# Kernel optimization log

Measured on AMD Instinct MI355X. Metric: run time of the kernel, lower is better.

Reference implementation:

```python
import jax, jax.numpy as jnp
import numpy as np

N_NODES = 50000
IN_DIM = 128
HIDDEN = 64
OUT_DIM = 3
HEADS1 = 4
NEG_SLOPE = 0.2
EPS = 1e-16


def _glorot(key, shape):
    fan_in, fan_out = shape[0], shape[-1]
    lim = (6.0 / (fan_in + fan_out)) ** 0.5
    return jax.random.uniform(key, shape, jnp.float32, -lim, lim)


def setup_inputs() -> dict:
    key = jax.random.key(0)
    ks = jax.random.split(key, 12)
    x = jax.random.normal(ks[0], (N_NODES, IN_DIM), jnp.float32)
    edge_index = jax.random.randint(ks[1], (2, 400000), 0, N_NODES, jnp.int64)
    # layer 1: GATConv(in=128, out=64, heads=4)
    W1 = _glorot(ks[2], (IN_DIM, HEADS1 * HIDDEN))
    att_src1 = _glorot(ks[3], (HEADS1, HIDDEN))
    att_dst1 = _glorot(ks[4], (HEADS1, HIDDEN))
    b1 = jnp.zeros((HEADS1 * HIDDEN,), jnp.float32)
    # layer 2: GATConv(in=256, out=64, heads=1)
    W2 = _glorot(ks[5], (HEADS1 * HIDDEN, HIDDEN))
    att_src2 = _glorot(ks[6], (1, HIDDEN))
    att_dst2 = _glorot(ks[7], (1, HIDDEN))
    b2 = jnp.zeros((HIDDEN,), jnp.float32)
    # output linear
    Wout = _glorot(ks[8], (HIDDEN, OUT_DIM))
    bout = jnp.zeros((OUT_DIM,), jnp.float32)
    return {"x": x, "edge_index": edge_index, "W1": W1, "att_src1": att_src1,
            "att_dst1": att_dst1, "b1": b1, "W2": W2, "att_src2": att_src2,
            "att_dst2": att_dst2, "b2": b2, "Wout": Wout, "bout": bout}


def gat_conv(x, src, dst, W, a_src, a_dst, b, n_nodes):
    H, C = a_src.shape
    h = (x @ W).reshape(n_nodes, H, C)            # [N,H,C]
    a_s = jnp.sum(h * a_src[None], axis=-1)        # [N,H]
    a_d = jnp.sum(h * a_dst[None], axis=-1)        # [N,H]
    e = jax.nn.leaky_relu(a_s[src] + a_d[dst], NEG_SLOPE)  # [E,H]
    # segment softmax over incoming edges of each dst node
    m = jax.ops.segment_max(e, dst, num_segments=n_nodes)
    ex = jnp.exp(e - m[dst])
    denom = jax.ops.segment_sum(ex, dst, num_segments=n_nodes)
    alpha = ex / (denom[dst] + EPS)                # [E,H]
    msg = h[src] * alpha[..., None]                # [E,H,C]
    out = jax.ops.segment_sum(msg, dst, num_segments=n_nodes)
    return out.reshape(n_nodes, H * C) + b


def reference(x, edge_index, W1, att_src1, att_dst1, b1, W2, att_src2, att_dst2, b2, Wout, bout):
    n = x.shape[0]
    loop = jnp.arange(n, dtype=edge_index.dtype)
    src = jnp.concatenate([edge_index[0], loop])   # add self loops (PyG default)
    dst = jnp.concatenate([edge_index[1], loop])
    h = gat_conv(x, src, dst, W1, att_src1, att_dst1, b1, n)
    h = jax.nn.elu(h)
    h = gat_conv(h, src, dst, W2, att_src2, att_dst2, b2, n)
    h = jax.nn.elu(h)
    return h @ Wout + bout
```

## Files before the change

kernel.cpp:

```cpp
#include <hip/hip_runtime.h>
#include <hip/hip_bf16.h>
#include <math.h>

#define N_NODES  50000
#define IN_DIM   128
#define HIDDEN   64
#define OUT_DIM  3
#define HEADS1   4
#define E_RAW    400000
#define E_TOT    450000
#define NEG_SLOPE 0.2f
#define WPREP_BLOCKS 128
#define EB_SC ((E_TOT + 255) / 256)
#define MB_GE (N_NODES / 16)

typedef __attribute__((ext_vector_type(8))) short bf16x8;
typedef __attribute__((ext_vector_type(4))) float f32x4;

static __device__ __forceinline__ float bfu(unsigned short u) {
    return __uint_as_float(((unsigned)u) << 16);
}
static __device__ __forceinline__ unsigned short f2b_bits(float v) {
    __hip_bfloat16 b = __float2bfloat16(v);
    return *reinterpret_cast<unsigned short*>(&b);
}

static __device__ __forceinline__ void get_edge(const int* __restrict__ ei, int is64,
                                                int e, int& s, int& d) {
    if (e >= E_RAW) { s = d = e - E_RAW; return; }
    if (is64) { s = ei[2 * e]; d = ei[2 * E_RAW + 2 * e]; }
    else      { s = ei[e];     d = ei[E_RAW + e]; }
    s = min(max(s, 0), N_NODES - 1);
    d = min(max(d, 0), N_NODES - 1);
}

static __device__ __forceinline__ int block_is64(const int* __restrict__ ei,
                                                 int e, bool valid, int* nzbuf) {
    bool real = valid && (e < E_RAW);
    int hv = real ? ei[2 * e + 1] : 0;
    if (threadIdx.x == 0) *nzbuf = 0;
    __syncthreads();
    if (__any(hv != 0) && (threadIdx.x & 63) == 0) *nzbuf = 1;
    __syncthreads();
    return (*nzbuf == 0);
}

__global__ void wprep_count_kernel(const float* __restrict__ W1, __hip_bfloat16* __restrict__ W1T,
                                   const float* __restrict__ W2, __hip_bfloat16* __restrict__ W2T,
                                   const int* __restrict__ ei, int* __restrict__ deg) {
    __shared__ int nz;
    int bid = blockIdx.x;
    if (bid < WPREP_BLOCKS) {
        int i = bid * 256 + threadIdx.x;
        if (i < 256 * 128) {
            int n = i >> 7, k = i & 127;
            *((unsigned short*)W1T + i) = f2b_bits(W1[k * 256 + n]);
        }
        if (i < 64 * 256) {
            int n = i >> 8, k = i & 255;
            *((unsigned short*)W2T + i) = f2b_bits(W2[k * 64 + n]);
        }
        return;
    }
    int e = (bid - WPREP_BLOCKS) * 256 + threadIdx.x;
    bool valid = e < E_TOT;
    int is64 = block_is64(ei, e, valid, &nz);
    if (!valid) return;
    int s, d;
    get_edge(ei, is64, e, s, d);
    atomicAdd(&deg[d], 1);
}

__global__ void scan_all_kernel(const int* __restrict__ deg, int* __restrict__ row_ptr,
                                int* __restrict__ cursor) {
    __shared__ int wsum[4];
    const int t = threadIdx.x, wv = t >> 6, ln = t & 63;
    int carry = 0;
    if (t == 0) row_ptr[0] = 0;
    for (int chunk = 0; chunk < 49; ++chunk) {
        int g = chunk * 256 + t;
        int4 d = (g < 12500) ? ((const int4*)deg)[g] : make_int4(0, 0, 0, 0);
        int p0 = d.x, p1 = p0 + d.y, p2 = p1 + d.z, p3 = p2 + d.w;
        int s = p3;
        #pragma unroll
        for (int off = 1; off < 64; off <<= 1) {
            int u = __shfl_up(s, off, 64);
            if (ln >= off) s += u;
        }
        if (ln == 63) wsum[wv] = s;
        __syncthreads();
        int wbase = carry;
        #pragma unroll
        for (int w = 0; w < 4; w++) wbase += (w < wv) ? wsum[w] : 0;
        int ex = wbase + s - p3;
        if (g < 12500) {
            int i = g * 4;
            row_ptr[i + 1] = ex + p0; row_ptr[i + 2] = ex + p1;
            row_ptr[i + 3] = ex + p2; row_ptr[i + 4] = ex + p3;
            cursor[i]     = ex;       cursor[i + 1]  = ex + p0;
            cursor[i + 2] = ex + p1;  cursor[i + 3]  = ex + p2;
        }
        carry += wsum[0] + wsum[1] + wsum[2] + wsum[3];
        __syncthreads();
    }
}

__global__ void __launch_bounds__(256) scatter_gemm_l1_kernel(
        const int* __restrict__ ei,
        int* __restrict__ cursor, int* __restrict__ csr_src,
        const float* __restrict__ x, const __hip_bfloat16* __restrict__ W1T,
        const float* __restrict__ att_s, const float* __restrict__ att_d,
        __hip_bfloat16* __restrict__ h1,
        float* __restrict__ asb4, float* __restrict__ adb4) {
    __shared__ unsigned short As[16][136];
    __shared__ int nz;
    if (blockIdx.x < EB_SC) {
        int e = blockIdx.x * 256 + threadIdx.x;
        bool valid = e < E_TOT;
        int is64 = block_is64(ei, e, valid, &nz);
        if (!valid) return;
        int s, d;
        get_edge(ei, is64, e, s, d);
        int pos = atomicAdd(&cursor[d], 1);
        csr_src[pos] = s;
        return;
    }
    const int tid = threadIdx.x;
    const int wave = tid >> 6, lane = tid & 63;
    const int quad = lane >> 4, m = lane & 15;
    const int row0 = (blockIdx.x - EB_SC) * 16;
    {
        int r = tid >> 4, seg = tid & 15;
        const float* xa = x + (size_t)(row0 + r) * IN_DIM + seg * 8;
        float4 u = *(const float4*)xa;
        float4 v = *(const float4*)(xa + 4);
        ushort4 p0, p1;
        p0.x = f2b_bits(u.x); p0.y = f2b_bits(u.y); p0.z = f2b_bits(u.z); p0.w = f2b_bits(u.w);
        p1.x = f2b_bits(v.x); p1.y = f2b_bits(v.y); p1.z = f2b_bits(v.z); p1.w = f2b_bits(v.w);
        *(ushort4*)&As[r][seg * 8]     = p0;
        *(ushort4*)&As[r][seg * 8 + 4] = p1;
    }
    __syncthreads();
    const int n0w = wave * 64;
    f32x4 acc0 = {0.f, 0.f, 0.f, 0.f}, acc1 = acc0, acc2 = acc0, acc3 = acc0;
    #pragma unroll
    for (int k0 = 0; k0 < IN_DIM; k0 += 32) {
        int kk = k0 + quad * 8;
        bf16x8 a = *(const bf16x8*)&As[m][kk];
        bf16x8 b0 = *(const bf16x8*)(W1T + (size_t)(n0w +  0 + m) * IN_DIM + kk);
        bf16x8 b1 = *(const bf16x8*)(W1T + (size_t)(n0w + 16 + m) * IN_DIM + kk);
        bf16x8 b2 = *(const bf16x8*)(W1T + (size_t)(n0w + 32 + m) * IN_DIM + kk);
        bf16x8 b3 = *(const bf16x8*)(W1T + (size_t)(n0w + 48 + m) * IN_DIM + kk);
        acc0 = __builtin_amdgcn_mfma_f32_16x16x32_bf16(a, b0, acc0, 0, 0, 0);
        acc1 = __builtin_amdgcn_mfma_f32_16x16x32_bf16(a, b1, acc1, 0, 0, 0);
        acc2 = __builtin_amdgcn_mfma_f32_16x16x32_bf16(a, b2, acc2, 0, 0, 0);
        acc3 = __builtin_amdgcn_mfma_f32_16x16x32_bf16(a, b3, acc3, 0, 0, 0);
    }
    float ats0 = att_s[n0w +  0 + m], atd0 = att_d[n0w +  0 + m];
    float ats1 = att_s[n0w + 16 + m], atd1 = att_d[n0w + 16 + m];
    float ats2 = att_s[n0w + 32 + m], atd2 = att_d[n0w + 32 + m];
    float ats3 = att_s[n0w + 48 + m], atd3 = att_d[n0w + 48 + m];
    unsigned short* out = (unsigned short*)h1;
    #pragma unroll
    for (int i = 0; i < 4; i++) {
        int grow = row0 + quad * 4 + i;
        size_t base = (size_t)grow * 256;
        out[base + n0w +  0 + m] = f2b_bits(acc0[i]);
        out[base + n0w + 16 + m] = f2b_bits(acc1[i]);
        out[base + n0w + 32 + m] = f2b_bits(acc2[i]);
        out[base + n0w + 48 + m] = f2b_bits(acc3[i]);
        float ps = acc0[i] * ats0 + acc1[i] * ats1 + acc2[i] * ats2 + acc3[i] * ats3;
        float pd = acc0[i] * atd0 + acc1[i] * atd1 + acc2[i] * atd2 + acc3[i] * atd3;
        #pragma unroll
        for (int off = 1; off < 16; off <<= 1) {
            ps += __shfl_xor(ps, off, 16);
            pd += __shfl_xor(pd, off, 16);
        }
        if (m == 0) {
            asb4[grow * 4 + wave] = ps;
            adb4[grow * 4 + wave] = pd;
        }
    }
}

__global__ void __launch_bounds__(256) gat_gather4_kernel(
        const int* __restrict__ row_ptr, const int* __restrict__ csr_src,
        const float* __restrict__ asb4, const float* __restrict__ adb4,
        const __hip_bfloat16* __restrict__ h1, const float* __restrict__ bias,
        __hip_bfloat16* __restrict__ eluagg) {
    int wave = threadIdx.x >> 6;
    int lane = threadIdx.x & 63;
    int n = blockIdx.x * 4 + wave;
    if (n >= N_NODES) return;
    int b = row_ptr[n], e = row_ptr[n + 1];
    const int c    = lane & 31;
    const int slot = lane >> 5;
    const int head = c >> 3;
    const int ei   = lane >> 2;
    const int hh   = lane & 3;
    float adnh = adb4[n * 4 + hh];
    float acc[8];
    #pragma unroll
    for (int i = 0; i < 8; i++) acc[i] = 0.f;
    float l = 0.f;
    for (int c0 = b; c0 < e; c0 += 16) {
        int cnt = min(16, e - c0);
        int s_all = (lane < cnt) ? csr_src[c0 + lane] : 0;
        int sE = __shfl(s_all, ei, 64);
        float w_all = 0.f;
        if (ei < cnt) {
            float v = asb4[sE * 4 + hh] + adnh;
            v = (v > 0.f) ? v : NEG_SLOPE * v;
            w_all = __expf(v);
        }
        #pragma unroll 2
        for (int k = 0; k < cnt; k += 2) {
            int eidx = k + slot;
            int s = __shfl(s_all, eidx, 64);
            float w = __shfl(w_all, eidx * 4 + head, 64);
            bf16x8 f = *(const bf16x8*)(h1 + (size_t)s * 256 + c * 8);
            l += w;
            #pragma unroll
            for (int i = 0; i < 8; i++)
                acc[i] += w * bfu((unsigned short)f[i]);
        }
    }
    #pragma unroll
    for (int i = 0; i < 8; i++) acc[i] += __shfl_xor(acc[i], 32, 64);
    l += __shfl_xor(l, 32, 64);
    if (lane < 32) {
        float il = 1.f / (l + 1e-16f);
        float4 b0 = *(const float4*)(bias + c * 8);
        float4 b1 = *(const float4*)(bias + c * 8 + 4);
        float r[8];
        r[0] = acc[0] * il + b0.x; r[1] = acc[1] * il + b0.y;
        r[2] = acc[2] * il + b0.z; r[3] = acc[3] * il + b0.w;
        r[4] = acc[4] * il + b1.x; r[5] = acc[5] * il + b1.y;
        r[6] = acc[6] * il + b1.z; r[7] = acc[7] * il + b1.w;
        bf16x8 st;
        #pragma unroll
        for (int i = 0; i < 8; i++) {
            float v = (r[i] > 0.f) ? r[i] : expm1f(r[i]);
            st[i] = (short)f2b_bits(v);
        }
        *(bf16x8*)(eluagg + (size_t)n * 256 + c * 8) = st;
    }
}

__global__ void __launch_bounds__(256) gemm_l2_mfma_kernel(
        const __hip_bfloat16* __restrict__ eluagg, const __hip_bfloat16* __restrict__ W2T,
        const float* __restrict__ att_s, const float* __restrict__ att_d,
        __hip_bfloat16* __restrict__ h2,
        float* __restrict__ asb, float* __restrict__ adb) {
    __shared__ float sPS[4][16];
    __shared__ float sPD[4][16];
    const int tid = threadIdx.x;
    const int wave = tid >> 6, lane = tid & 63;
    const int quad = lane >> 4, m = lane & 15;
    const int row0 = blockIdx.x * 16;
    const int n0 = wave * 16;
    f32x4 acc = {0.f, 0.f, 0.f, 0.f};
    #pragma unroll
    for (int k0 = 0; k0 < 256; k0 += 32) {
        int kk = k0 + quad * 8;
        bf16x8 a = *(const bf16x8*)(eluagg + (size_t)(row0 + m) * 256 + kk);
        bf16x8 b = *(const bf16x8*)(W2T + (size_t)(n0 + m) * 256 + kk);
        acc = __builtin_amdgcn_mfma_f32_16x16x32_bf16(a, b, acc, 0, 0, 0);
    }
    float ats = att_s[n0 + m], atd = att_d[n0 + m];
    unsigned short* out = (unsigned short*)h2;
    #pragma unroll
    for (int i = 0; i < 4; i++) {
        int grow = row0 + quad * 4 + i;
        out[(size_t)grow * 64 + n0 + m] = f2b_bits(acc[i]);
        float ps = acc[i] * ats;
        float pd = acc[i] * atd;
        #pragma unroll
        for (int off = 1; off < 16; off <<= 1) {
            ps += __shfl_xor(ps, off, 16);
            pd += __shfl_xor(pd, off, 16);
        }
        if (m == 0) {
            sPS[wave][quad * 4 + i] = ps;
            sPD[wave][quad * 4 + i] = pd;
        }
    }
    __syncthreads();
    if (tid < 16) {
        float ps = sPS[0][tid] + sPS[1][tid] + sPS[2][tid] + sPS[3][tid];
        float pd = sPD[0][tid] + sPD[1][tid] + sPD[2][tid] + sPD[3][tid];
        asb[row0 + tid] = ps;
        adb[row0 + tid] = pd;
    }
}

__global__ void __launch_bounds__(256) gat_gather1_out_kernel(
        const int* __restrict__ row_ptr, const int* __restrict__ csr_src,
        const float* __restrict__ asb, const float* __restrict__ adb,
        const __hip_bfloat16* __restrict__ h2, const float* __restrict__ bias,
        const float* __restrict__ Wout, const float* __restrict__ bout,
        float* __restrict__ out) {
    int wave = threadIdx.x >> 6;
    int lane = threadIdx.x & 63;
    int n = blockIdx.x * 4 + wave;
    if (n >= N_NODES) return;
    int b = row_ptr[n], e = row_ptr[n + 1];
    const int c    = lane & 7;
    const int slot = lane >> 3;
    float adn = adb[n];
    float acc[8];
    #pragma unroll
    for (int i = 0; i < 8; i++) acc[i] = 0.f;
    float l = 0.f;
    for (int c0 = b; c0 < e; c0 += 64) {
        int cnt = min(64, e - c0);
        int s_all = (lane < cnt) ? csr_src[c0 + lane] : 0;
        float w_all = 0.f;
        if (lane < cnt) {
            float v = asb[s_all] + adn;
            v = (v > 0.f) ? v : NEG_SLOPE * v;
            w_all = __expf(v);
        }
        #pragma unroll 2
        for (int k = 0; k < cnt; k += 8) {
            int eidx = k + slot;
            int s = __shfl(s_all, eidx, 64);
            float w = __shfl(w_all, eidx, 64);
            bf16x8 f = *(const bf16x8*)(h2 + (size_t)s * 64 + c * 8);
            l += w;
            #pragma unroll
            for (int i = 0; i < 8; i++)
                acc[i] += w * bfu((unsigned short)f[i]);
        }
    }
    #pragma unroll
    for (int off = 8; off < 64; off <<= 1) {
        #pragma unroll
        for (int i = 0; i < 8; i++) acc[i] += __shfl_xor(acc[i], off, 64);
        l += __shfl_xor(l, off, 64);
    }
    float il = 1.f / (l + 1e-16f);
    float4 b0 = *(const float4*)(bias + c * 8);
    float4 b1 = *(const float4*)(bias + c * 8 + 4);
    float v[8];
    v[0] = acc[0] * il + b0.x; v[1] = acc[1] * il + b0.y;
    v[2] = acc[2] * il + b0.z; v[3] = acc[3] * il + b0.w;
    v[4] = acc[4] * il + b1.x; v[5] = acc[5] * il + b1.y;
    v[6] = acc[6] * il + b1.z; v[7] = acc[7] * il + b1.w;
    #pragma unroll
    for (int i = 0; i < 8; i++) v[i] = (v[i] > 0.f) ? v[i] : expm1f(v[i]);
    const float* wp = Wout + c * 24;
    float o0 = 0.f, o1 = 0.f, o2 = 0.f;
    #pragma unroll
    for (int i = 0; i < 8; i++) {
        o0 += v[i] * wp[i * 3 + 0];
        o1 += v[i] * wp[i * 3 + 1];
        o2 += v[i] * wp[i * 3 + 2];
    }
    #pragma unroll
    for (int off = 1; off < 8; off <<= 1) {
        o0 += __shfl_xor(o0, off, 64);
        o1 += __shfl_xor(o1, off, 64);
        o2 += __shfl_xor(o2, off, 64);
    }
    if (lane == 0) {
        out[n * OUT_DIM + 0] = o0 + bout[0];
        out[n * OUT_DIM + 1] = o1 + bout[1];
        out[n * OUT_DIM + 2] = o2 + bout[2];
    }
}

extern "C" void kernel_launch(void* const* d_in, const int* in_sizes, int n_in,
                              void* d_out, int out_size, void* d_ws, size_t ws_size,
                              hipStream_t stream) {
    const float* x    = (const float*)d_in[0];
    const int*   ei   = (const int*)d_in[1];
    const float* W1   = (const float*)d_in[2];
    const float* as1  = (const float*)d_in[3];
    const float* ad1  = (const float*)d_in[4];
    const float* b1   = (const float*)d_in[5];
    const float* W2   = (const float*)d_in[6];
    const float* as2  = (const float*)d_in[7];
    const float* ad2  = (const float*)d_in[8];
    const float* b2v  = (const float*)d_in[9];
    const float* Wout = (const float*)d_in[10];
    const float* bout = (const float*)d_in[11];
    float* out = (float*)d_out;

    float* ws    = (float*)d_ws;
    float* asb4  = ws + 16;
    float* adb4  = asb4 + (size_t)N_NODES * 4;
    float* asb1  = adb4 + (size_t)N_NODES * 4;
    float* adb1  = asb1 + N_NODES;
    __hip_bfloat16* h1     = (__hip_bfloat16*)(adb1 + N_NODES);
    __hip_bfloat16* eluagg = (__hip_bfloat16*)(h1 + (size_t)N_NODES * 256);
    __hip_bfloat16* h2     = (__hip_bfloat16*)(eluagg + (size_t)N_NODES * 256);
    __hip_bfloat16* W1T    = (__hip_bfloat16*)(h2 + (size_t)N_NODES * 64);
    __hip_bfloat16* W2T    = W1T + 256 * 128;
    int* deg     = (int*)(W2T + 64 * 256);
    int* row_ptr = deg + N_NODES;
    int* cursor  = row_ptr + N_NODES + 16;
    int* csr_src = cursor + N_NODES;

    const int EB = EB_SC;
    const int AB = (N_NODES + 3) / 4;

    hipMemsetAsync(deg, 0, (size_t)N_NODES * sizeof(int), stream);
    wprep_count_kernel<<<WPREP_BLOCKS + EB, 256, 0, stream>>>(W1, W1T, W2, W2T, ei, deg);
    scan_all_kernel<<<1, 256, 0, stream>>>(deg, row_ptr, cursor);

    scatter_gemm_l1_kernel<<<EB + MB_GE, 256, 0, stream>>>(ei, cursor, csr_src,
                                                           x, W1T, as1, ad1, h1, asb4, adb4);

    gat_gather4_kernel<<<AB, 256, 0, stream>>>(row_ptr, csr_src, asb4, adb4, h1, b1, eluagg);

    gemm_l2_mfma_kernel<<<MB_GE, 256, 0, stream>>>(eluagg, W2T, as2, ad2, h2, asb1, adb1);

    gat_gather1_out_kernel<<<AB, 256, 0, stream>>>(row_ptr, csr_src, asb1, adb1, h2,
                                                   b2v, Wout, bout, out);
}
```

Baseline: 297.3 us.

## Fuse layer-1 gather with layer-2 GEMM, parallelize scan, stage GEMM stores in LDS

Layer-1 attention aggregation and the layer-2 MFMA GEMM now run in one 1024-thread kernel: 16 waves each aggregate one node into LDS, then four waves run the GEMM from LDS. This removes the round trip of the 50000x256 bf16 eluagg buffer through global memory. The single-block prefix scan becomes a 49-block scan where each block re-sums the earlier degree chunks, and both GEMM epilogues stage results in LDS so they can be written with coalesced 16-byte stores. The cost is larger blocks, a barrier per block and idle waves during the GEMM phase.

```diff
diff --git a/kernel.cpp b/kernel.cpp
--- a/kernel.cpp
+++ b/kernel.cpp
@@ -10,6 +10,7 @@
 #define E_RAW    400000
 #define E_TOT    450000
 #define NEG_SLOPE 0.2f
+#define N_CHUNKS 49
 #define WPREP_BLOCKS 128
 #define EB_SC ((E_TOT + 255) / 256)
 #define MB_GE (N_NODES / 16)
@@ -71,38 +72,47 @@
     atomicAdd(&deg[d], 1);
 }
 
-__global__ void scan_all_kernel(const int* __restrict__ deg, int* __restrict__ row_ptr,
-                                int* __restrict__ cursor) {
+__global__ void scan_fused_kernel(const int* __restrict__ deg, int* __restrict__ row_ptr,
+                                  int* __restrict__ cursor) {
     __shared__ int wsum[4];
-    const int t = threadIdx.x, wv = t >> 6, ln = t & 63;
-    int carry = 0;
-    if (t == 0) row_ptr[0] = 0;
-    for (int chunk = 0; chunk < 49; ++chunk) {
-        int g = chunk * 256 + t;
-        int4 d = (g < 12500) ? ((const int4*)deg)[g] : make_int4(0, 0, 0, 0);
-        int p0 = d.x, p1 = p0 + d.y, p2 = p1 + d.z, p3 = p2 + d.w;
-        int s = p3;
-        #pragma unroll
-        for (int off = 1; off < 64; off <<= 1) {
-            int u = __shfl_up(s, off, 64);
-            if (ln >= off) s += u;
-        }
-        if (ln == 63) wsum[wv] = s;
-        __syncthreads();
-        int wbase = carry;
-        #pragma unroll
-        for (int w = 0; w < 4; w++) wbase += (w < wv) ? wsum[w] : 0;
-        int ex = wbase + s - p3;
-        if (g < 12500) {
-            int i = g * 4;
-            row_ptr[i + 1] = ex + p0; row_ptr[i + 2] = ex + p1;
-            row_ptr[i + 3] = ex + p2; row_ptr[i + 4] = ex + p3;
-            cursor[i]     = ex;       cursor[i + 1]  = ex + p0;
-            cursor[i + 2] = ex + p1;  cursor[i + 3]  = ex + p2;
-        }
-        carry += wsum[0] + wsum[1] + wsum[2] + wsum[3];
-        __syncthreads();
-    }
+    __shared__ int sbase;
+    const int bid = blockIdx.x, t = threadIdx.x, wv = t >> 6, ln = t & 63;
+    int base = 0;
+    const int ng = bid * 256;
+    for (int g = t; g < ng; g += 256) {
+        int4 d = ((const int4*)deg)[g];
+        base += (d.x + d.y) + (d.z + d.w);
+    }
+    #pragma unroll
+    for (int off = 1; off < 64; off <<= 1) base += __shfl_xor(base, off, 64);
+    if (ln == 0) wsum[wv] = base;
+    __syncthreads();
+    if (t == 0) sbase = wsum[0] + wsum[1] + wsum[2] + wsum[3];
+    __syncthreads();
+    base = sbase;
+    int g = bid * 256 + t;
+    int4 d = (g < 12500) ? ((const int4*)deg)[g] : make_int4(0, 0, 0, 0);
+    int p0 = d.x, p1 = p0 + d.y, p2 = p1 + d.z, p3 = p2 + d.w;
+    int s = p3;
+    #pragma unroll
+    for (int off = 1; off < 64; off <<= 1) {
+        int u = __shfl_up(s, off, 64);
+        if (ln >= off) s += u;
+    }
+    if (ln == 63) wsum[wv] = s;
+    __syncthreads();
+    int wbase = base;
+    #pragma unroll
+    for (int w = 0; w < 4; w++) wbase += (w < wv) ? wsum[w] : 0;
+    int ex = wbase + s - p3;
+    if (g < 12500) {
+        int i = g * 4;
+        row_ptr[i + 1] = ex + p0; row_ptr[i + 2] = ex + p1;
+        row_ptr[i + 3] = ex + p2; row_ptr[i + 4] = ex + p3;
+        cursor[i]     = ex;       cursor[i + 1]  = ex + p0;
+        cursor[i + 2] = ex + p1;  cursor[i + 3]  = ex + p2;
+    }
+    if (bid == 0 && t == 0) row_ptr[0] = 0;
 }
 
 __global__ void __launch_bounds__(256) scatter_gemm_l1_kernel(
@@ -113,6 +123,7 @@
         __hip_bfloat16* __restrict__ h1,
         float* __restrict__ asb4, float* __restrict__ adb4) {
     __shared__ unsigned short As[16][136];
+    __shared__ __attribute__((aligned(16))) unsigned short hT[16][264];
     __shared__ int nz;
     if (blockIdx.x < EB_SC) {
         int e = blockIdx.x * 256 + threadIdx.x;
@@ -160,15 +171,13 @@
     float ats1 = att_s[n0w + 16 + m], atd1 = att_d[n0w + 16 + m];
     float ats2 = att_s[n0w + 32 + m], atd2 = att_d[n0w + 32 + m];
     float ats3 = att_s[n0w + 48 + m], atd3 = att_d[n0w + 48 + m];
-    unsigned short* out = (unsigned short*)h1;
     #pragma unroll
     for (int i = 0; i < 4; i++) {
-        int grow = row0 + quad * 4 + i;
-        size_t base = (size_t)grow * 256;
-        out[base + n0w +  0 + m] = f2b_bits(acc0[i]);
-        out[base + n0w + 16 + m] = f2b_bits(acc1[i]);
-        out[base + n0w + 32 + m] = f2b_bits(acc2[i]);
-        out[base + n0w + 48 + m] = f2b_bits(acc3[i]);
+        int r = quad * 4 + i;
+        hT[r][n0w +  0 + m] = f2b_bits(acc0[i]);
+        hT[r][n0w + 16 + m] = f2b_bits(acc1[i]);
+        hT[r][n0w + 32 + m] = f2b_bits(acc2[i]);
+        hT[r][n0w + 48 + m] = f2b_bits(acc3[i]);
         float ps = acc0[i] * ats0 + acc1[i] * ats1 + acc2[i] * ats2 + acc3[i] * ats3;
         float pd = acc0[i] * atd0 + acc1[i] * atd1 + acc2[i] * atd2 + acc3[i] * atd3;
         #pragma unroll
@@ -177,115 +186,130 @@
             pd += __shfl_xor(pd, off, 16);
         }
         if (m == 0) {
-            asb4[grow * 4 + wave] = ps;
-            adb4[grow * 4 + wave] = pd;
-        }
-    }
-}
-
-__global__ void __launch_bounds__(256) gat_gather4_kernel(
+            asb4[(row0 + r) * 4 + wave] = ps;
+            adb4[(row0 + r) * 4 + wave] = pd;
+        }
+    }
+    __syncthreads();
+    {
+        unsigned short* hrow = (unsigned short*)h1;
+        int r0 = tid >> 5, c0 = tid & 31;
+        *(bf16x8*)(hrow + (size_t)(row0 + r0) * 256 + c0 * 8) = *(const bf16x8*)&hT[r0][c0 * 8];
+        int S = tid + 256;
+        int r1 = S >> 5, c1 = S & 31;
+        *(bf16x8*)(hrow + (size_t)(row0 + r1) * 256 + c1 * 8) = *(const bf16x8*)&hT[r1][c1 * 8];
+    }
+}
+
+__global__ void __launch_bounds__(1024, 8) gat_gather4_l2_kernel(
         const int* __restrict__ row_ptr, const int* __restrict__ csr_src,
         const float* __restrict__ asb4, const float* __restrict__ adb4,
         const __hip_bfloat16* __restrict__ h1, const float* __restrict__ bias,
-        __hip_bfloat16* __restrict__ eluagg) {
-    int wave = threadIdx.x >> 6;
-    int lane = threadIdx.x & 63;
-    int n = blockIdx.x * 4 + wave;
-    if (n >= N_NODES) return;
-    int b = row_ptr[n], e = row_ptr[n + 1];
-    const int c    = lane & 31;
-    const int slot = lane >> 5;
-    const int head = c >> 3;
-    const int ei   = lane >> 2;
-    const int hh   = lane & 3;
-    float adnh = adb4[n * 4 + hh];
-    float acc[8];
-    #pragma unroll
-    for (int i = 0; i < 8; i++) acc[i] = 0.f;
-    float l = 0.f;
-    for (int c0 = b; c0 < e; c0 += 16) {
-        int cnt = min(16, e - c0);
-        int s_all = (lane < cnt) ? csr_src[c0 + lane] : 0;
-        int sE = __shfl(s_all, ei, 64);
-        float w_all = 0.f;
-        if (ei < cnt) {
-            float v = asb4[sE * 4 + hh] + adnh;
-            v = (v > 0.f) ? v : NEG_SLOPE * v;
-            w_all = __expf(v);
-        }
-        #pragma unroll 2
-        for (int k = 0; k < cnt; k += 2) {
-            int eidx = k + slot;
-            int s = __shfl(s_all, eidx, 64);
-            float w = __shfl(w_all, eidx * 4 + head, 64);
-            bf16x8 f = *(const bf16x8*)(h1 + (size_t)s * 256 + c * 8);
-            l += w;
-            #pragma unroll
-            for (int i = 0; i < 8; i++)
-                acc[i] += w * bfu((unsigned short)f[i]);
-        }
-    }
-    #pragma unroll
-    for (int i = 0; i < 8; i++) acc[i] += __shfl_xor(acc[i], 32, 64);
-    l += __shfl_xor(l, 32, 64);
-    if (lane < 32) {
-        float il = 1.f / (l + 1e-16f);
-        float4 b0 = *(const float4*)(bias + c * 8);
-        float4 b1 = *(const float4*)(bias + c * 8 + 4);
-        float r[8];
-        r[0] = acc[0] * il + b0.x; r[1] = acc[1] * il + b0.y;
-        r[2] = acc[2] * il + b0.z; r[3] = acc[3] * il + b0.w;
-        r[4] = acc[4] * il + b1.x; r[5] = acc[5] * il + b1.y;
-        r[6] = acc[6] * il + b1.z; r[7] = acc[7] * il + b1.w;
-        bf16x8 st;
-        #pragma unroll
-        for (int i = 0; i < 8; i++) {
-            float v = (r[i] > 0.f) ? r[i] : expm1f(r[i]);
-            st[i] = (short)f2b_bits(v);
-        }
-        *(bf16x8*)(eluagg + (size_t)n * 256 + c * 8) = st;
-    }
-}
-
-__global__ void __launch_bounds__(256) gemm_l2_mfma_kernel(
-        const __hip_bfloat16* __restrict__ eluagg, const __hip_bfloat16* __restrict__ W2T,
+        const __hip_bfloat16* __restrict__ W2T,
         const float* __restrict__ att_s, const float* __restrict__ att_d,
         __hip_bfloat16* __restrict__ h2,
         float* __restrict__ asb, float* __restrict__ adb) {
+    __shared__ __attribute__((aligned(16))) unsigned short As[16][264];
+    __shared__ __attribute__((aligned(16))) unsigned short hT2[16][72];
     __shared__ float sPS[4][16];
     __shared__ float sPD[4][16];
     const int tid = threadIdx.x;
     const int wave = tid >> 6, lane = tid & 63;
-    const int quad = lane >> 4, m = lane & 15;
     const int row0 = blockIdx.x * 16;
-    const int n0 = wave * 16;
-    f32x4 acc = {0.f, 0.f, 0.f, 0.f};
-    #pragma unroll
-    for (int k0 = 0; k0 < 256; k0 += 32) {
-        int kk = k0 + quad * 8;
-        bf16x8 a = *(const bf16x8*)(eluagg + (size_t)(row0 + m) * 256 + kk);
-        bf16x8 b = *(const bf16x8*)(W2T + (size_t)(n0 + m) * 256 + kk);
-        acc = __builtin_amdgcn_mfma_f32_16x16x32_bf16(a, b, acc, 0, 0, 0);
-    }
-    float ats = att_s[n0 + m], atd = att_d[n0 + m];
-    unsigned short* out = (unsigned short*)h2;
-    #pragma unroll
-    for (int i = 0; i < 4; i++) {
-        int grow = row0 + quad * 4 + i;
-        out[(size_t)grow * 64 + n0 + m] = f2b_bits(acc[i]);
-        float ps = acc[i] * ats;
-        float pd = acc[i] * atd;
-        #pragma unroll
-        for (int off = 1; off < 16; off <<= 1) {
-            ps += __shfl_xor(ps, off, 16);
-            pd += __shfl_xor(pd, off, 16);
-        }
-        if (m == 0) {
-            sPS[wave][quad * 4 + i] = ps;
-            sPD[wave][quad * 4 + i] = pd;
-        }
-    }
-    __syncthreads();
+    const int c    = lane & 31;
+    const int slot = lane >> 5;
+    const int head = c >> 3;
+    const int eidx0 = lane >> 2;
+    const int hh   = lane & 3;
+
+    {
+        const int n = row0 + wave;
+        int b = row_ptr[n], e = row_ptr[n + 1];
+        float adnh = adb4[n * 4 + hh];
+        float acc[8];
+        #pragma unroll
+        for (int i = 0; i < 8; i++) acc[i] = 0.f;
+        float l = 0.f;
+        for (int c0 = b; c0 < e; c0 += 16) {
+            int cnt = min(16, e - c0);
+            int s_all = (lane < cnt) ? csr_src[c0 + lane] : 0;
+            int sE = __shfl(s_all, eidx0, 64);
+            float w_all = 0.f;
+            if (eidx0 < cnt) {
+                float v = asb4[sE * 4 + hh] + adnh;
+                v = (v > 0.f) ? v : NEG_SLOPE * v;
+                w_all = __expf(v);
+            }
+            #pragma unroll 2
+            for (int k = 0; k < cnt; k += 2) {
+                int eidx = k + slot;
+                int s = __shfl(s_all, eidx, 64);
+                float w = __shfl(w_all, eidx * 4 + head, 64);
+                bf16x8 f = *(const bf16x8*)(h1 + (size_t)s * 256 + c * 8);
+                l += w;
+                #pragma unroll
+                for (int i = 0; i < 8; i++)
+                    acc[i] += w * bfu((unsigned short)f[i]);
+            }
+        }
+        #pragma unroll
+        for (int i = 0; i < 8; i++) acc[i] += __shfl_xor(acc[i], 32, 64);
+        l += __shfl_xor(l, 32, 64);
+        if (lane < 32) {
+            float il = 1.f / (l + 1e-16f);
+            float4 b0 = *(const float4*)(bias + c * 8);
+            float4 b1 = *(const float4*)(bias + c * 8 + 4);
+            float r[8];
+            r[0] = acc[0] * il + b0.x; r[1] = acc[1] * il + b0.y;
+            r[2] = acc[2] * il + b0.z; r[3] = acc[3] * il + b0.w;
+            r[4] = acc[4] * il + b1.x; r[5] = acc[5] * il + b1.y;
+            r[6] = acc[6] * il + b1.z; r[7] = acc[7] * il + b1.w;
+            bf16x8 st;
+            #pragma unroll
+            for (int i = 0; i < 8; i++) {
+                float v = (r[i] > 0.f) ? r[i] : expm1f(r[i]);
+                st[i] = (short)f2b_bits(v);
+            }
+            *(bf16x8*)&As[wave][c * 8] = st;
+        }
+    }
+    __syncthreads();
+
+    if (wave < 4) {
+        const int quad = lane >> 4, m = lane & 15;
+        const int n0 = wave * 16;
+        f32x4 acc = {0.f, 0.f, 0.f, 0.f};
+        #pragma unroll
+        for (int k0 = 0; k0 < 256; k0 += 32) {
+            int kk = k0 + quad * 8;
+            bf16x8 a = *(const bf16x8*)&As[m][kk];
+            bf16x8 bfr = *(const bf16x8*)(W2T + (size_t)(n0 + m) * 256 + kk);
+            acc = __builtin_amdgcn_mfma_f32_16x16x32_bf16(a, bfr, acc, 0, 0, 0);
+        }
+        float ats = att_s[n0 + m], atd = att_d[n0 + m];
+        #pragma unroll
+        for (int i = 0; i < 4; i++) {
+            int r = quad * 4 + i;
+            hT2[r][n0 + m] = f2b_bits(acc[i]);
+            float ps = acc[i] * ats;
+            float pd = acc[i] * atd;
+            #pragma unroll
+            for (int off = 1; off < 16; off <<= 1) {
+                ps += __shfl_xor(ps, off, 16);
+                pd += __shfl_xor(pd, off, 16);
+            }
+            if (m == 0) {
+                sPS[wave][r] = ps;
+                sPD[wave][r] = pd;
+            }
+        }
+    }
+    __syncthreads();
+    if (tid < 128) {
+        int r = tid >> 3, cs = tid & 7;
+        *(bf16x8*)((unsigned short*)h2 + (size_t)(row0 + r) * 64 + cs * 8) =
+            *(const bf16x8*)&hT2[r][cs * 8];
+    }
     if (tid < 16) {
         float ps = sPS[0][tid] + sPS[1][tid] + sPS[2][tid] + sPS[3][tid];
         float pd = sPD[0][tid] + sPD[1][tid] + sPD[2][tid] + sPD[3][tid];
@@ -393,8 +417,7 @@
     float* asb1  = adb4 + (size_t)N_NODES * 4;
     float* adb1  = asb1 + N_NODES;
     __hip_bfloat16* h1     = (__hip_bfloat16*)(adb1 + N_NODES);
-    __hip_bfloat16* eluagg = (__hip_bfloat16*)(h1 + (size_t)N_NODES * 256);
-    __hip_bfloat16* h2     = (__hip_bfloat16*)(eluagg + (size_t)N_NODES * 256);
+    __hip_bfloat16* h2     = (__hip_bfloat16*)(h1 + (size_t)N_NODES * 256);
     __hip_bfloat16* W1T    = (__hip_bfloat16*)(h2 + (size_t)N_NODES * 64);
     __hip_bfloat16* W2T    = W1T + 256 * 128;
     int* deg     = (int*)(W2T + 64 * 256);
@@ -407,14 +430,13 @@
 
     hipMemsetAsync(deg, 0, (size_t)N_NODES * sizeof(int), stream);
     wprep_count_kernel<<<WPREP_BLOCKS + EB, 256, 0, stream>>>(W1, W1T, W2, W2T, ei, deg);
-    scan_all_kernel<<<1, 256, 0, stream>>>(deg, row_ptr, cursor);
+    scan_fused_kernel<<<N_CHUNKS, 256, 0, stream>>>(deg, row_ptr, cursor);
 
     scatter_gemm_l1_kernel<<<EB + MB_GE, 256, 0, stream>>>(ei, cursor, csr_src,
                                                            x, W1T, as1, ad1, h1, asb4, adb4);
 
-    gat_gather4_kernel<<<AB, 256, 0, stream>>>(row_ptr, csr_src, asb4, adb4, h1, b1, eluagg);
-
-    gemm_l2_mfma_kernel<<<MB_GE, 256, 0, stream>>>(eluagg, W2T, as2, ad2, h2, asb1, adb1);
+    gat_gather4_l2_kernel<<<MB_GE, 1024, 0, stream>>>(row_ptr, csr_src, asb4, adb4, h1, b1,
+                                                      W2T, as2, ad2, h2, asb1, adb1);
 
     gat_gather1_out_kernel<<<AB, 256, 0, stream>>>(row_ptr, csr_src, asb1, adb1, h2,
                                                    b2v, Wout, bout, out);
```

Result: faster. 260.9 us, median of 2 (-12.3%).
